# Kernel tuning notes

Measured on AMD Instinct MI355X. Metric: run time of the kernel, lower is better.

The kernel has to match this reference:

```python
import jax, jax.numpy as jnp
import numpy as np
import math

EMBED = 1024
HEADS = 16
HEAD_DIM = 64
HIDDEN = 4 * EMBED
EPS = 1e-5


def setup_inputs() -> dict:
    key = jax.random.key(0)
    ks = jax.random.split(key, 12)
    B, T, C = 2, 2048, EMBED
    s = 0.02
    return {
        "x": jax.random.normal(ks[0], (B, T, C), jnp.float32),
        "ln1_g": jnp.ones((C,), jnp.float32),
        "ln1_b": jnp.zeros((C,), jnp.float32),
        "qkv_w": jax.random.normal(ks[1], (C, 3 * C), jnp.float32) * s,
        "qkv_b": jnp.zeros((3 * C,), jnp.float32),
        "out_w": jax.random.normal(ks[2], (C, C), jnp.float32) * s,
        "out_b": jnp.zeros((C,), jnp.float32),
        "ln2_g": jnp.ones((C,), jnp.float32),
        "ln2_b": jnp.zeros((C,), jnp.float32),
        "fc1_w": jax.random.normal(ks[3], (C, HIDDEN), jnp.float32) * s,
        "fc1_b": jnp.zeros((HIDDEN,), jnp.float32),
        "fc2_w": jax.random.normal(ks[4], (HIDDEN, C), jnp.float32) * s,
        "fc2_b": jnp.zeros((C,), jnp.float32),
    }


def _layernorm(x, g, b):
    mu = jnp.mean(x, axis=-1, keepdims=True)
    var = jnp.var(x, axis=-1, keepdims=True)
    return (x - mu) * jax.lax.rsqrt(var + EPS) * g + b


def _attention(x, qkv_w, qkv_b, out_w, out_b):
    B, T, C = x.shape
    qkv = x @ qkv_w + qkv_b  # [B,T,3C]
    q, k, v = jnp.split(qkv, 3, axis=-1)
    # [B,H,T,hd]
    def heads(t):
        return t.reshape(B, T, HEADS, HEAD_DIM).transpose(0, 2, 1, 3)
    q, k, v = heads(q), heads(k), heads(v)
    scale = 1.0 / math.sqrt(HEAD_DIM)
    attn = jnp.einsum('bhqd,bhkd->bhqk', q, k) * scale
    causal = jnp.triu(jnp.ones((T, T), bool), k=1)
    attn = jnp.where(causal, -jnp.inf, attn)
    attn = jax.nn.softmax(attn, axis=-1)
    out = jnp.einsum('bhqk,bhkd->bhqd', attn, v)
    out = out.transpose(0, 2, 1, 3).reshape(B, T, C)
    return out @ out_w + out_b


def reference(x, ln1_g, ln1_b, qkv_w, qkv_b, out_w, out_b, ln2_g, ln2_b, fc1_w, fc1_b, fc2_w, fc2_b):
    x = x + _attention(_layernorm(x, ln1_g, ln1_b), qkv_w, qkv_b, out_w, out_b)
    h = _layernorm(x, ln2_g, ln2_b)
    h = jax.nn.gelu(h @ fc1_w + fc1_b, approximate=False) @ fc2_w + fc2_b
    return x + h
```

## Files before the change

kernel.cpp:

```cpp
#include <hip/hip_runtime.h>
#include <hip/hip_bf16.h>
#include <math.h>

typedef float f32x4 __attribute__((ext_vector_type(4)));
typedef __bf16 bf16x8 __attribute__((ext_vector_type(8)));
typedef __hip_bfloat16 bf16;

constexpr int T_SEQ = 2048;
constexpr int C_EMB = 1024;
constexpr int N_HEAD = 16;
constexpr int D_HEAD = 64;
constexpr int BATCH = 2;
constexpr int M_ROWS = BATCH * T_SEQ;
constexpr int HIDDEN_DIM = 4096;

static __device__ __forceinline__ f32x4 zero4() {
  f32x4 z; z[0] = 0.f; z[1] = 0.f; z[2] = 0.f; z[3] = 0.f; return z;
}

static __device__ __forceinline__ void gl_lds16(const bf16* g, bf16* l) {
  __builtin_amdgcn_global_load_lds(
      (const __attribute__((address_space(1))) unsigned int*)g,
      (__attribute__((address_space(3))) unsigned int*)l, 16, 0, 0);
}

__global__ __launch_bounds__(256) void ln_kernel(const float* __restrict__ x,
                                                 const float* __restrict__ gamma,
                                                 const float* __restrict__ beta,
                                                 bf16* __restrict__ out) {
  int row = blockIdx.x;
  const float* xr = x + (size_t)row * C_EMB;
  int t = threadIdx.x;
  float4 v = *(const float4*)&xr[t * 4];
  float s = v.x + v.y + v.z + v.w;
  float ss = v.x * v.x + v.y * v.y + v.z * v.z + v.w * v.w;
#pragma unroll
  for (int off = 32; off > 0; off >>= 1) {
    s += __shfl_down(s, off, 64);
    ss += __shfl_down(ss, off, 64);
  }
  __shared__ float sbuf[8];
  int w = t >> 6;
  if ((t & 63) == 0) { sbuf[w] = s; sbuf[4 + w] = ss; }
  __syncthreads();
  s = sbuf[0] + sbuf[1] + sbuf[2] + sbuf[3];
  ss = sbuf[4] + sbuf[5] + sbuf[6] + sbuf[7];
  float mu = s * (1.0f / C_EMB);
  float var = ss * (1.0f / C_EMB) - mu * mu;
  float rstd = rsqrtf(var + 1e-5f);
  float4 g4 = *(const float4*)&gamma[t * 4];
  float4 b4 = *(const float4*)&beta[t * 4];
  bf16* orow = out + (size_t)row * C_EMB + t * 4;
  orow[0] = __float2bfloat16((v.x - mu) * rstd * g4.x + b4.x);
  orow[1] = __float2bfloat16((v.y - mu) * rstd * g4.y + b4.y);
  orow[2] = __float2bfloat16((v.z - mu) * rstd * g4.z + b4.z);
  orow[3] = __float2bfloat16((v.w - mu) * rstd * g4.w + b4.w);
}

__global__ __launch_bounds__(256) void ln_red(const float* __restrict__ p0,
                                              const float* __restrict__ p1,
                                              const float* __restrict__ bias,
                                              const float* __restrict__ res,
                                              const float* __restrict__ gamma,
                                              const float* __restrict__ beta,
                                              float* __restrict__ x2,
                                              bf16* __restrict__ xb) {
  int row = blockIdx.x;
  int t = threadIdx.x;
  size_t base = (size_t)row * C_EMB + t * 4;
  float4 a = *(const float4*)&p0[base];
  float4 b = *(const float4*)&p1[base];
  float4 r = *(const float4*)&res[base];
  float4 bi = *(const float4*)&bias[t * 4];
  float4 v;
  v.x = a.x + b.x + r.x + bi.x;
  v.y = a.y + b.y + r.y + bi.y;
  v.z = a.z + b.z + r.z + bi.z;
  v.w = a.w + b.w + r.w + bi.w;
  *(float4*)&x2[base] = v;
  float s = v.x + v.y + v.z + v.w;
  float ss = v.x * v.x + v.y * v.y + v.z * v.z + v.w * v.w;
#pragma unroll
  for (int off = 32; off > 0; off >>= 1) {
    s += __shfl_down(s, off, 64);
    ss += __shfl_down(ss, off, 64);
  }
  __shared__ float sbuf[8];
  int w = t >> 6;
  if ((t & 63) == 0) { sbuf[w] = s; sbuf[4 + w] = ss; }
  __syncthreads();
  s = sbuf[0] + sbuf[1] + sbuf[2] + sbuf[3];
  ss = sbuf[4] + sbuf[5] + sbuf[6] + sbuf[7];
  float mu = s * (1.0f / C_EMB);
  float var = ss * (1.0f / C_EMB) - mu * mu;
  float rstd = rsqrtf(var + 1e-5f);
  float4 g4 = *(const float4*)&gamma[t * 4];
  float4 b4 = *(const float4*)&beta[t * 4];
  bf16* orow = xb + base;
  orow[0] = __float2bfloat16((v.x - mu) * rstd * g4.x + b4.x);
  orow[1] = __float2bfloat16((v.y - mu) * rstd * g4.y + b4.y);
  orow[2] = __float2bfloat16((v.z - mu) * rstd * g4.z + b4.z);
  orow[3] = __float2bfloat16((v.w - mu) * rstd * g4.w + b4.w);
}

__global__ __launch_bounds__(256) void cast_transpose(const float* __restrict__ src,
                                                      bf16* __restrict__ dst,
                                                      int K, int N) {
  __shared__ float tile[32][33];
  int n0 = blockIdx.x * 32, k0 = blockIdx.y * 32;
  int tx = threadIdx.x & 31, ty = threadIdx.x >> 5;
#pragma unroll
  for (int i = 0; i < 4; ++i)
    tile[ty + 8 * i][tx] = src[(size_t)(k0 + ty + 8 * i) * N + n0 + tx];
  __syncthreads();
#pragma unroll
  for (int i = 0; i < 4; ++i)
    dst[(size_t)(n0 + ty + 8 * i) * K + k0 + tx] = __float2bfloat16(tile[tx][ty + 8 * i]);
}

__global__ __launch_bounds__(256) void transpose_v(const bf16* __restrict__ V,
                                                   bf16* __restrict__ Vt) {
  int tt = blockIdx.x, bh = blockIdx.y;
  __shared__ bf16 tile[64][72];
  const bf16* src = V + ((size_t)bh * T_SEQ + tt * 64) * 64;
  int t = threadIdx.x;
  for (int idx = t; idx < 512; idx += 256) {
    int r = idx >> 3, c = (idx & 7) * 8;
    *(int4*)&tile[r][c] = *(const int4*)&src[r * 64 + c];
  }
  __syncthreads();
  bf16* dst = Vt + ((size_t)bh * 64) * T_SEQ + tt * 64;
  for (int idx = t; idx < 512; idx += 256) {
    int d = idx >> 3, c = (idx & 7) * 8;
    union { bf16 h[8]; int4 v; } u;
#pragma unroll
    for (int j = 0; j < 8; ++j) u.h[j] = tile[c + j][d];
    *(int4*)&dst[(size_t)d * T_SEQ + c] = u.v;
  }
}

template <int EPI, int BN>
__global__ __launch_bounds__(512) void gemm256(
    const bf16* __restrict__ A, const bf16* __restrict__ Bt,
    const float* __restrict__ bias, int M, int N, int K, int ksplit,
    bf16* __restrict__ out_b16,
    bf16* __restrict__ q_out, bf16* __restrict__ k_out, bf16* __restrict__ v_out,
    float* __restrict__ part0, float* __restrict__ part1) {
  constexpr int NFR = BN / 64;
  constexpr int NB = BN / 64;
  __shared__ bf16 Abuf[2][256 * 64];
  __shared__ bf16 Bbuf[2][BN * 64];

  int gx = gridDim.x, nwg = gx * gridDim.y;
  int flat = blockIdx.y * gx + blockIdx.x;
  int swz = (flat & 7) * (nwg >> 3) + (flat >> 3);
  int bx = swz % gx, by = swz / gx;

  int m0 = by * 256, n0 = bx * BN;
  int t = threadIdx.x;
  int wv = t >> 6, lane = t & 63, g = lane >> 4, r16 = lane & 15;
  int wm = wv >> 2, wn = wv & 3;

  f32x4 acc[8][NFR];
#pragma unroll
  for (int i = 0; i < 8; ++i)
#pragma unroll
    for (int j = 0; j < NFR; ++j) acc[i][j] = zero4();

  int srow = wv * 8 + (lane >> 3);
  int srcg = (lane & 7) ^ (lane >> 3);

  int klen = K / ksplit;
  int kbeg = blockIdx.z * klen;
  int NT = klen / 64;

  const bf16* gAp[4];
  const bf16* gBp[NB];
#pragma unroll
  for (int i = 0; i < 4; ++i)
    gAp[i] = A + (size_t)(m0 + i * 64 + srow) * K + kbeg + srcg * 8;
#pragma unroll
  for (int i = 0; i < NB; ++i)
    gBp[i] = Bt + (size_t)(n0 + i * 64 + srow) * K + kbeg + srcg * 8;

  int aoff[8], boff[NFR], xk[2];
#pragma unroll
  for (int mi = 0; mi < 8; ++mi) aoff[mi] = (wm * 128 + mi * 16 + r16) * 64;
#pragma unroll
  for (int ni = 0; ni < NFR; ++ni) boff[ni] = (wn * NFR * 16 + ni * 16 + r16) * 64;
#pragma unroll
  for (int kk = 0; kk < 2; ++kk) xk[kk] = (((kk * 4 + g) ^ (r16 & 7)) << 3);

  auto stage = [&](int buf) {
#pragma unroll
    for (int i = 0; i < 4; ++i) {
      gl_lds16(gAp[i], &Abuf[buf][(i * 64 + wv * 8) * 64]);
      gAp[i] += 64;
    }
#pragma unroll
    for (int i = 0; i < NB; ++i) {
      gl_lds16(gBp[i], &Bbuf[buf][(i * 64 + wv * 8) * 64]);
      gBp[i] += 64;
    }
  };

  auto compute = [&](int buf) {
    const bf16* Ab = &Abuf[buf][0];
    const bf16* Bb = &Bbuf[buf][0];
    bf16x8 bfr[NFR][2];
#pragma unroll
    for (int ni = 0; ni < NFR; ++ni)
#pragma unroll
      for (int kk = 0; kk < 2; ++kk)
        bfr[ni][kk] = *(const bf16x8*)&Bb[boff[ni] + xk[kk]];
    bf16x8 aa[2][2];
#pragma unroll
    for (int kk = 0; kk < 2; ++kk) aa[0][kk] = *(const bf16x8*)&Ab[aoff[0] + xk[kk]];
#pragma unroll
    for (int mi = 0; mi < 8; ++mi) {
      if (mi + 1 < 8) {
#pragma unroll
        for (int kk = 0; kk < 2; ++kk)
          aa[(mi + 1) & 1][kk] = *(const bf16x8*)&Ab[aoff[mi + 1] + xk[kk]];
      }
#pragma unroll
      for (int ni = 0; ni < NFR; ++ni) {
        acc[mi][ni] = __builtin_amdgcn_mfma_f32_16x16x32_bf16(aa[mi & 1][0], bfr[ni][0], acc[mi][ni], 0, 0, 0);
        acc[mi][ni] = __builtin_amdgcn_mfma_f32_16x16x32_bf16(aa[mi & 1][1], bfr[ni][1], acc[mi][ni], 0, 0, 0);
      }
    }
  };

  stage(0);
  __syncthreads();
  for (int tt = 0; tt < NT; ++tt) {
    int cur = tt & 1;
    if (tt + 1 < NT) stage(cur ^ 1);
    compute(cur);
    __syncthreads();
  }

  float* pout = (EPI == 3) ? (blockIdx.z == 0 ? part0 : part1) : nullptr;

#pragma unroll
  for (int mi = 0; mi < 8; ++mi) {
#pragma unroll
    for (int ni = 0; ni < NFR; ++ni) {
      int col = n0 + wn * NFR * 16 + ni * 16 + r16;
      float bv = (EPI == 3) ? 0.0f : bias[col];
#pragma unroll
      for (int reg = 0; reg < 4; ++reg) {
        int row = m0 + wm * 128 + mi * 16 + g * 4 + reg;
        float v = acc[mi][ni][reg] + bv;
        if constexpr (EPI == 0) {
          int part = col >> 10, cc = col & 1023;
          int hh = cc >> 6, dd = cc & 63;
          int bb = row >> 11, tt2 = row & 2047;
          size_t idx = (((size_t)bb * N_HEAD + hh) * T_SEQ + tt2) * D_HEAD + dd;
          if (part == 0) q_out[idx] = __float2bfloat16(v * 0.125f);
          else if (part == 1) k_out[idx] = __float2bfloat16(v);
          else v_out[idx] = __float2bfloat16(v);
        } else if constexpr (EPI == 2) {
          float ge = 0.5f * v * (1.0f + erff(v * 0.70710678118f));
          out_b16[(size_t)row * N + col] = __float2bfloat16(ge);
        } else {
          pout[(size_t)row * N + col] = v;
        }
      }
    }
  }
}

__global__ __launch_bounds__(256) void reduce_add(const float* __restrict__ p0,
                                                  const float* __restrict__ p1,
                                                  const float* __restrict__ bias,
                                                  const float* __restrict__ res,
                                                  float* __restrict__ out,
                                                  int total, int N) {
  for (int i = (blockIdx.x * 256 + threadIdx.x) * 4; i < total; i += gridDim.x * 1024) {
    float4 a = *(const float4*)&p0[i];
    float4 b = *(const float4*)&p1[i];
    float4 r = *(const float4*)&res[i];
    float4 bi = *(const float4*)&bias[i & (N - 1)];
    float4 o;
    o.x = a.x + b.x + r.x + bi.x;
    o.y = a.y + b.y + r.y + bi.y;
    o.z = a.z + b.z + r.z + bi.z;
    o.w = a.w + b.w + r.w + bi.w;
    *(float4*)&out[i] = o;
  }
}

__global__ __launch_bounds__(256) void attn_kernel(const bf16* __restrict__ Q,
                                                   const bf16* __restrict__ Kg,
                                                   const bf16* __restrict__ Vt,
                                                   bf16* __restrict__ O) {
  constexpr int NQ = T_SEQ / 64;
  int p = blockIdx.x, bh = blockIdx.y;
  int qtA = p, qtB = NQ - 1 - p;
  int b = bh >> 4, h = bh & 15;
  __shared__ bf16 Ks[2][64 * 64];
  __shared__ bf16 Vs[2][64 * 64];
  __shared__ bf16 Ps[4][16 * 64];
  int t = threadIdx.x, w = t >> 6, lane = t & 63, g = lane >> 4, r16 = lane & 15;

  const bf16* QpA = Q + ((size_t)bh * T_SEQ + qtA * 64) * 64;
  const bf16* QpB = Q + ((size_t)bh * T_SEQ + qtB * 64) * 64;
  bf16x8 qfA[2], qfB[2];
#pragma unroll
  for (int kk = 0; kk < 2; ++kk) {
    qfA[kk] = *(const bf16x8*)&QpA[(w * 16 + r16) * 64 + kk * 32 + g * 8];
    qfB[kk] = *(const bf16x8*)&QpB[(w * 16 + r16) * 64 + kk * 32 + g * 8];
  }

  float lsA[4] = {0.f, 0.f, 0.f, 0.f}, lsB[4] = {0.f, 0.f, 0.f, 0.f};
  f32x4 oA[4], oB[4];
#pragma unroll
  for (int i = 0; i < 4; ++i) { oA[i] = zero4(); oB[i] = zero4(); }

  bf16* Psw = Ps[w];

  int sg0 = w * 128 + lane, sg1 = w * 128 + 64 + lane;
  int sr0 = sg0 >> 3, sc0 = (sg0 & 7) ^ (sr0 & 7);
  int sr1 = sg1 >> 3, sc1 = (sg1 & 7) ^ (sr1 & 7);

  auto stage = [&](int kt, int buf) {
    const bf16* Kp = Kg + ((size_t)bh * T_SEQ + kt * 64) * 64;
    const bf16* Vp = Vt + (size_t)bh * 64 * T_SEQ + kt * 64;
    gl_lds16(Kp + sr0 * 64 + sc0 * 8, &Ks[buf][(w * 128) * 8]);
    gl_lds16(Vp + (size_t)sr0 * T_SEQ + sc0 * 8, &Vs[buf][(w * 128) * 8]);
    gl_lds16(Kp + sr1 * 64 + sc1 * 8, &Ks[buf][(w * 128 + 64) * 8]);
    gl_lds16(Vp + (size_t)sr1 * T_SEQ + sc1 * 8, &Vs[buf][(w * 128 + 64) * 8]);
  };

  auto process = [&](const bf16x8* qf, float* ls, f32x4* o_acc, bool diag,
                     const bf16* Ksb, const bf16* Vsb) {
    f32x4 s[4];
#pragma unroll
    for (int ni = 0; ni < 4; ++ni) {
      s[ni] = zero4();
#pragma unroll
      for (int kk = 0; kk < 2; ++kk) {
        bf16x8 kf = *(const bf16x8*)&Ksb[(ni * 16 + r16) * 64 + (((kk * 4 + g) ^ (r16 & 7)) << 3)];
        s[ni] = __builtin_amdgcn_mfma_f32_16x16x32_bf16(qf[kk], kf, s[ni], 0, 0, 0);
      }
    }
    if (diag) {
#pragma unroll
      for (int ni = 0; ni < 4; ++ni) {
        int kl = ni * 16 + r16;
#pragma unroll
        for (int reg = 0; reg < 4; ++reg) {
          int ql = w * 16 + g * 4 + reg;
          if (kl > ql) s[ni][reg] = -1e30f;
        }
      }
    }
#pragma unroll
    for (int ni = 0; ni < 4; ++ni) {
#pragma unroll
      for (int reg = 0; reg < 4; ++reg) {
        float pv = __expf(s[ni][reg]);
        s[ni][reg] = pv;
        ls[reg] += pv;
        int rr = g * 4 + reg;
        Psw[rr * 64 + (((ni * 2 + (r16 >> 3)) ^ (rr & 7)) << 3) + (r16 & 7)] =
            __float2bfloat16(pv);
      }
    }
    bf16x8 pf[2];
#pragma unroll
    for (int kk = 0; kk < 2; ++kk)
      pf[kk] = *(const bf16x8*)&Psw[r16 * 64 + (((kk * 4 + g) ^ (r16 & 7)) << 3)];
#pragma unroll
    for (int nd = 0; nd < 4; ++nd)
#pragma unroll
      for (int kk = 0; kk < 2; ++kk) {
        bf16x8 vf = *(const bf16x8*)&Vsb[(nd * 16 + r16) * 64 + (((kk * 4 + g) ^ (r16 & 7)) << 3)];
        o_acc[nd] = __builtin_amdgcn_mfma_f32_16x16x32_bf16(pf[kk], vf, o_acc[nd], 0, 0, 0);
      }
  };

  stage(0, 0);
  __syncthreads();
  for (int kt = 0; kt <= qtB; ++kt) {
    int cur = kt & 1;
    if (kt + 1 <= qtB) stage(kt + 1, cur ^ 1);
    process(qfB, lsB, oB, kt == qtB, &Ks[cur][0], &Vs[cur][0]);
    if (kt <= qtA) process(qfA, lsA, oA, kt == qtA, &Ks[cur][0], &Vs[cur][0]);
    __syncthreads();
  }

#pragma unroll
  for (int reg = 0; reg < 4; ++reg) {
#pragma unroll
    for (int off = 1; off < 16; off <<= 1) {
      lsA[reg] += __shfl_xor(lsA[reg], off, 64);
      lsB[reg] += __shfl_xor(lsB[reg], off, 64);
    }
  }
#pragma unroll
  for (int reg = 0; reg < 4; ++reg) {
    float invA = 1.0f / lsA[reg];
    float invB = 1.0f / lsB[reg];
    int rowA = b * T_SEQ + qtA * 64 + w * 16 + g * 4 + reg;
    int rowB = b * T_SEQ + qtB * 64 + w * 16 + g * 4 + reg;
#pragma unroll
    for (int nd = 0; nd < 4; ++nd) {
      int col = h * 64 + nd * 16 + r16;
      O[(size_t)rowA * C_EMB + col] = __float2bfloat16(oA[nd][reg] * invA);
      O[(size_t)rowB * C_EMB + col] = __float2bfloat16(oB[nd][reg] * invB);
    }
  }
}

extern "C" void kernel_launch(void* const* d_in, const int* in_sizes, int n_in,
                              void* d_out, int out_size, void* d_ws, size_t ws_size,
                              hipStream_t stream) {
  (void)in_sizes; (void)n_in; (void)out_size; (void)ws_size;
  const float* x     = (const float*)d_in[0];
  const float* ln1_g = (const float*)d_in[1];
  const float* ln1_b = (const float*)d_in[2];
  const float* qkv_w = (const float*)d_in[3];
  const float* qkv_b = (const float*)d_in[4];
  const float* out_w = (const float*)d_in[5];
  const float* out_b = (const float*)d_in[6];
  const float* ln2_g = (const float*)d_in[7];
  const float* ln2_b = (const float*)d_in[8];
  const float* fc1_w = (const float*)d_in[9];
  const float* fc1_b = (const float*)d_in[10];
  const float* fc2_w = (const float*)d_in[11];
  const float* fc2_b = (const float*)d_in[12];
  float* out = (float*)d_out;

  char* ws = (char*)d_ws;
  size_t off = 0;
  auto alloc = [&](size_t bytes) {
    void* p = ws + off;
    off += (bytes + 255) & ~(size_t)255;
    return p;
  };
  bf16* Wqkv = (bf16*)alloc((size_t)3 * C_EMB * C_EMB * 2);
  bf16* Wout = (bf16*)alloc((size_t)C_EMB * C_EMB * 2);
  bf16* W1   = (bf16*)alloc((size_t)HIDDEN_DIM * C_EMB * 2);
  bf16* W2   = (bf16*)alloc((size_t)C_EMB * HIDDEN_DIM * 2);
  float* x2  = (float*)alloc((size_t)M_ROWS * C_EMB * 4);
  bf16* Xb   = (bf16*)alloc((size_t)M_ROWS * C_EMB * 2);
  bf16* Qb   = (bf16*)alloc((size_t)M_ROWS * C_EMB * 2 * 4);
  bf16* Kb   = Qb + (size_t)M_ROWS * C_EMB;
  bf16* Vb   = Kb + (size_t)M_ROWS * C_EMB;
  bf16* Vtb  = Vb + (size_t)M_ROWS * C_EMB;
  bf16* H1   = Qb;
  float* p0o = (float*)Qb;
  float* p1o = (float*)Vb;
  float* p0f = (float*)Wqkv;
  float* p1f = (float*)alloc((size_t)M_ROWS * C_EMB * 4);

  cast_transpose<<<dim3(3 * C_EMB / 32, C_EMB / 32), 256, 0, stream>>>(qkv_w, Wqkv, C_EMB, 3 * C_EMB);
  cast_transpose<<<dim3(C_EMB / 32, C_EMB / 32), 256, 0, stream>>>(out_w, Wout, C_EMB, C_EMB);
  cast_transpose<<<dim3(HIDDEN_DIM / 32, C_EMB / 32), 256, 0, stream>>>(fc1_w, W1, C_EMB, HIDDEN_DIM);
  cast_transpose<<<dim3(C_EMB / 32, HIDDEN_DIM / 32), 256, 0, stream>>>(fc2_w, W2, HIDDEN_DIM, C_EMB);

  ln_kernel<<<M_ROWS, 256, 0, stream>>>(x, ln1_g, ln1_b, Xb);

  gemm256<0, 256><<<dim3(3 * C_EMB / 256, M_ROWS / 256), 512, 0, stream>>>(
      Xb, Wqkv, qkv_b, M_ROWS, 3 * C_EMB, C_EMB, 1,
      nullptr, Qb, Kb, Vb, nullptr, nullptr);

  transpose_v<<<dim3(T_SEQ / 64, BATCH * N_HEAD), 256, 0, stream>>>(Vb, Vtb);

  attn_kernel<<<dim3(T_SEQ / 128, BATCH * N_HEAD), 256, 0, stream>>>(Qb, Kb, Vtb, Xb);

  gemm256<3, 128><<<dim3(C_EMB / 128, M_ROWS / 256, 2), 512, 0, stream>>>(
      Xb, Wout, nullptr, M_ROWS, C_EMB, C_EMB, 2,
      nullptr, nullptr, nullptr, nullptr, p0o, p1o);
  ln_red<<<M_ROWS, 256, 0, stream>>>(p0o, p1o, out_b, x, ln2_g, ln2_b, x2, Xb);

  gemm256<2, 256><<<dim3(HIDDEN_DIM / 256, M_ROWS / 256), 512, 0, stream>>>(
      Xb, W1, fc1_b, M_ROWS, HIDDEN_DIM, C_EMB, 1,
      H1, nullptr, nullptr, nullptr, nullptr, nullptr);

  gemm256<3, 128><<<dim3(C_EMB / 128, M_ROWS / 256, 2), 512, 0, stream>>>(
      H1, W2, nullptr, M_ROWS, C_EMB, HIDDEN_DIM, 2,
      nullptr, nullptr, nullptr, nullptr, p0f, p1f);
  reduce_add<<<2048, 256, 0, stream>>>(p0f, p1f, fc2_b, x2, out,
                                       M_ROWS * C_EMB, C_EMB);
}
```

Before: 243.7 us.

## Use explicit vmcnt waits and split barriers to overlap prefetch with compute

Replaces the __syncthreads-based double-buffer loops in the GEMM and attention kernels with raw s_barrier calls, sched_barrier fences, and s_waitcnt vmcnt(N). This lets the next tile's global-to-LDS loads stay in flight while the current tile is computed, instead of draining every outstanding load at each barrier. It also raises wave priority during GEMM compute. The risk is correctness: the vmcnt counts must exactly match the number of loads issued per stage, or data races on LDS can occur.

Measured after the change: 254.7 us. +4.5%, slower.

```diff
diff --git a/kernel.cpp b/kernel.cpp
--- a/kernel.cpp
+++ b/kernel.cpp
@@ -148,6 +148,7 @@
     float* __restrict__ part0, float* __restrict__ part1) {
   constexpr int NFR = BN / 64;
   constexpr int NB = BN / 64;
+  constexpr int LOADS = 4 + NB;
   __shared__ bf16 Abuf[2][256 * 64];
   __shared__ bf16 Bbuf[2][BN * 64];
 
@@ -232,12 +233,22 @@
   };
 
   stage(0);
-  __syncthreads();
   for (int tt = 0; tt < NT; ++tt) {
     int cur = tt & 1;
-    if (tt + 1 < NT) stage(cur ^ 1);
+    __builtin_amdgcn_s_barrier();
+    __builtin_amdgcn_sched_barrier(0);
+    if (tt + 1 < NT) {
+      stage(cur ^ 1);
+      asm volatile("s_waitcnt vmcnt(%0)" :: "n"(LOADS) : "memory");
+    } else {
+      asm volatile("s_waitcnt vmcnt(0)" ::: "memory");
+    }
+    __builtin_amdgcn_sched_barrier(0);
+    __builtin_amdgcn_s_barrier();
+    __builtin_amdgcn_sched_barrier(0);
+    __builtin_amdgcn_s_setprio(1);
     compute(cur);
-    __syncthreads();
+    __builtin_amdgcn_s_setprio(0);
   }
 
   float* pout = (EPI == 3) ? (blockIdx.z == 0 ? part0 : part1) : nullptr;
@@ -382,13 +393,21 @@
   };
 
   stage(0, 0);
-  __syncthreads();
   for (int kt = 0; kt <= qtB; ++kt) {
     int cur = kt & 1;
-    if (kt + 1 <= qtB) stage(kt + 1, cur ^ 1);
+    __builtin_amdgcn_s_barrier();
+    __builtin_amdgcn_sched_barrier(0);
+    if (kt + 1 <= qtB) {
+      stage(kt + 1, cur ^ 1);
+      asm volatile("s_waitcnt vmcnt(4)" ::: "memory");
+    } else {
+      asm volatile("s_waitcnt vmcnt(0)" ::: "memory");
+    }
+    __builtin_amdgcn_sched_barrier(0);
+    __builtin_amdgcn_s_barrier();
+    __builtin_amdgcn_sched_barrier(0);
     process(qfB, lsB, oB, kt == qtB, &Ks[cur][0], &Vs[cur][0]);
     if (kt <= qtA) process(qfA, lsA, oA, kt == qtA, &Ks[cur][0], &Vs[cur][0]);
-    __syncthreads();
   }
 
 #pragma unroll
```

## Restructure GEMM into 8-phase half-tile pipeline with fine-grained barriers

Applied to the files above, without the earlier changes.

Replaces the double-buffered GEMM main loop with an 8-phase schedule. A and B tiles are split into halves that are staged one at a time, interleaved with MFMA sub-blocks, and guarded by explicit vmcnt waits and raw s_barrier. s_setprio is raised around the MFMA bursts. The goal is to overlap global-to-LDS loads with compute more evenly and to cut full-tile sync stalls. The cost is more barriers, and correctness now relies on the exact vmcnt counts.

After: 276.3 us. 13.4% more time.

```diff
diff --git a/kernel.cpp b/kernel.cpp
--- a/kernel.cpp
+++ b/kernel.cpp
@@ -23,6 +23,8 @@
       (const __attribute__((address_space(1))) unsigned int*)g,
       (__attribute__((address_space(3))) unsigned int*)l, 16, 0, 0);
 }
+
+#define BAR() asm volatile("s_barrier" ::: "memory")
 
 __global__ __launch_bounds__(256) void ln_kernel(const float* __restrict__ x,
                                                  const float* __restrict__ gamma,
@@ -140,16 +142,16 @@
 }
 
 template <int EPI, int BN>
-__global__ __launch_bounds__(512) void gemm256(
+__global__ __launch_bounds__(512) void gemm8p(
     const bf16* __restrict__ A, const bf16* __restrict__ Bt,
     const float* __restrict__ bias, int M, int N, int K, int ksplit,
     bf16* __restrict__ out_b16,
     bf16* __restrict__ q_out, bf16* __restrict__ k_out, bf16* __restrict__ v_out,
     float* __restrict__ part0, float* __restrict__ part1) {
   constexpr int NFR = BN / 64;
-  constexpr int NB = BN / 64;
-  __shared__ bf16 Abuf[2][256 * 64];
-  __shared__ bf16 Bbuf[2][BN * 64];
+  constexpr int BH = BN / 2;
+  __shared__ bf16 Asl[2][2][128 * 64];
+  __shared__ bf16 Bsl[2][2][BH * 64];
 
   int gx = gridDim.x, nwg = gx * gridDim.y;
   int flat = blockIdx.y * gx + blockIdx.x;
@@ -167,77 +169,93 @@
 #pragma unroll
     for (int j = 0; j < NFR; ++j) acc[i][j] = zero4();
 
-  int srow = wv * 8 + (lane >> 3);
-  int srcg = (lane & 7) ^ (lane >> 3);
+  int lrow8 = lane >> 3;
+  int srcg = (lane & 7) ^ lrow8;
 
   int klen = K / ksplit;
   int kbeg = blockIdx.z * klen;
   int NT = klen / 64;
-
-  const bf16* gAp[4];
-  const bf16* gBp[NB];
-#pragma unroll
-  for (int i = 0; i < 4; ++i)
-    gAp[i] = A + (size_t)(m0 + i * 64 + srow) * K + kbeg + srcg * 8;
-#pragma unroll
-  for (int i = 0; i < NB; ++i)
-    gBp[i] = Bt + (size_t)(n0 + i * 64 + srow) * K + kbeg + srcg * 8;
-
-  int aoff[8], boff[NFR], xk[2];
-#pragma unroll
-  for (int mi = 0; mi < 8; ++mi) aoff[mi] = (wm * 128 + mi * 16 + r16) * 64;
-#pragma unroll
-  for (int ni = 0; ni < NFR; ++ni) boff[ni] = (wn * NFR * 16 + ni * 16 + r16) * 64;
+  int NI = NT / 2;
+
+  auto stageA = [&](int tile, int h) {
+    int par = tile & 1;
+    const bf16* base = A + (size_t)(m0 + h * 128) * K + kbeg + tile * 64;
+#pragma unroll
+    for (int j = 0; j < 2; ++j) {
+      const bf16* src = base + (size_t)((wv * 2 + j) * 8 + lrow8) * K + srcg * 8;
+      gl_lds16(src, &Asl[par][h][((wv * 2 + j) * 8) * 64]);
+    }
+  };
+  auto stageB = [&](int tile, int h) {
+    int par = tile & 1;
+    const bf16* base = Bt + (size_t)(n0 + h * BH) * K + kbeg + tile * 64;
+    if constexpr (BN == 256) {
+#pragma unroll
+      for (int j = 0; j < 2; ++j) {
+        const bf16* src = base + (size_t)((wv * 2 + j) * 8 + lrow8) * K + srcg * 8;
+        gl_lds16(src, &Bsl[par][h][((wv * 2 + j) * 8) * 64]);
+      }
+    } else {
+      const bf16* src = base + (size_t)(wv * 8 + lrow8) * K + srcg * 8;
+      gl_lds16(src, &Bsl[par][h][(wv * 8) * 64]);
+    }
+  };
+
+  int xk[2];
 #pragma unroll
   for (int kk = 0; kk < 2; ++kk) xk[kk] = (((kk * 4 + g) ^ (r16 & 7)) << 3);
-
-  auto stage = [&](int buf) {
-#pragma unroll
-    for (int i = 0; i < 4; ++i) {
-      gl_lds16(gAp[i], &Abuf[buf][(i * 64 + wv * 8) * 64]);
-      gAp[i] += 64;
-    }
-#pragma unroll
-    for (int i = 0; i < NB; ++i) {
-      gl_lds16(gBp[i], &Bbuf[buf][(i * 64 + wv * 8) * 64]);
-      gBp[i] += 64;
-    }
-  };
-
-  auto compute = [&](int buf) {
-    const bf16* Ab = &Abuf[buf][0];
-    const bf16* Bb = &Bbuf[buf][0];
-    bf16x8 bfr[NFR][2];
-#pragma unroll
-    for (int ni = 0; ni < NFR; ++ni)
-#pragma unroll
-      for (int kk = 0; kk < 2; ++kk)
-        bfr[ni][kk] = *(const bf16x8*)&Bb[boff[ni] + xk[kk]];
-    bf16x8 aa[2][2];
-#pragma unroll
-    for (int kk = 0; kk < 2; ++kk) aa[0][kk] = *(const bf16x8*)&Ab[aoff[0] + xk[kk]];
-#pragma unroll
-    for (int mi = 0; mi < 8; ++mi) {
-      if (mi + 1 < 8) {
+  int bhalf = wn >> 1;
+  int blrow0 = (wn & 1) * 16 * NFR;
+
+  stageA(0, 0); stageA(0, 1); stageB(0, 0); stageB(0, 1);
+
+  bf16x8 bfr[NFR][2];
+
+  for (int it = 0; it < NI; ++it) {
+    int e = 2 * it, o = 2 * it + 1;
+#pragma unroll
+    for (int p = 0; p < 8; ++p) {
+      int stile = (p < 4) ? o : (e + 2);
+      int sh = p & 3;
+      bool staged = (stile < NT);
+      if (staged) {
+        if (sh < 2) stageA(stile, sh); else stageB(stile, sh - 2);
+      }
+      if ((p & 3) == 0) {
+        if (staged)
+          asm volatile("s_waitcnt vmcnt(2)" ::: "memory");
+        else
+          asm volatile("s_waitcnt vmcnt(0)" ::: "memory");
+        BAR();
+      }
+      int par = (p < 4) ? 0 : 1;
+      int q = p & 3;
+      const bf16* Ab = &Asl[par][wm][0];
+      const bf16* Bb = &Bsl[par][bhalf][0];
+      __builtin_amdgcn_s_setprio(1);
+      if (q == 0) {
+#pragma unroll
+        for (int ni = 0; ni < NFR; ++ni)
+#pragma unroll
+          for (int kk = 0; kk < 2; ++kk)
+            bfr[ni][kk] = *(const bf16x8*)&Bb[(blrow0 + ni * 16 + r16) * 64 + xk[kk]];
+      }
+      bf16x8 af[2][2];
+#pragma unroll
+      for (int d = 0; d < 2; ++d)
 #pragma unroll
         for (int kk = 0; kk < 2; ++kk)
-          aa[(mi + 1) & 1][kk] = *(const bf16x8*)&Ab[aoff[mi + 1] + xk[kk]];
-      }
-#pragma unroll
-      for (int ni = 0; ni < NFR; ++ni) {
-        acc[mi][ni] = __builtin_amdgcn_mfma_f32_16x16x32_bf16(aa[mi & 1][0], bfr[ni][0], acc[mi][ni], 0, 0, 0);
-        acc[mi][ni] = __builtin_amdgcn_mfma_f32_16x16x32_bf16(aa[mi & 1][1], bfr[ni][1], acc[mi][ni], 0, 0, 0);
-      }
-    }
-  };
-
-  stage(0);
-  __syncthreads();
-  for (int tt = 0; tt < NT; ++tt) {
-    int cur = tt & 1;
-    if (tt + 1 < NT) stage(cur ^ 1);
-    compute(cur);
-    __syncthreads();
+          af[d][kk] = *(const bf16x8*)&Ab[((2 * q + d) * 16 + r16) * 64 + xk[kk]];
+#pragma unroll
+      for (int d = 0; d < 2; ++d)
+#pragma unroll
+        for (int ni = 0; ni < NFR; ++ni) {
+          acc[2 * q + d][ni] = __builtin_amdgcn_mfma_f32_16x16x32_bf16(af[d][0], bfr[ni][0], acc[2 * q + d][ni], 0, 0, 0);
+          acc[2 * q + d][ni] = __builtin_amdgcn_mfma_f32_16x16x32_bf16(af[d][1], bfr[ni][1], acc[2 * q + d][ni], 0, 0, 0);
+        }
+      __builtin_amdgcn_s_setprio(0);
+      BAR();
+    }
   }
 
   float* pout = (EPI == 3) ? (blockIdx.z == 0 ? part0 : part1) : nullptr;
@@ -463,7 +481,7 @@
 
   ln_kernel<<<M_ROWS, 256, 0, stream>>>(x, ln1_g, ln1_b, Xb);
 
-  gemm256<0, 256><<<dim3(3 * C_EMB / 256, M_ROWS / 256), 512, 0, stream>>>(
+  gemm8p<0, 256><<<dim3(3 * C_EMB / 256, M_ROWS / 256), 512, 0, stream>>>(
       Xb, Wqkv, qkv_b, M_ROWS, 3 * C_EMB, C_EMB, 1,
       nullptr, Qb, Kb, Vb, nullptr, nullptr);
 
@@ -471,16 +489,16 @@
 
   attn_kernel<<<dim3(T_SEQ / 128, BATCH * N_HEAD), 256, 0, stream>>>(Qb, Kb, Vtb, Xb);
 
-  gemm256<3, 128><<<dim3(C_EMB / 128, M_ROWS / 256, 2), 512, 0, stream>>>(
+  gemm8p<3, 128><<<dim3(C_EMB / 128, M_ROWS / 256, 2), 512, 0, stream>>>(
       Xb, Wout, nullptr, M_ROWS, C_EMB, C_EMB, 2,
       nullptr, nullptr, nullptr, nullptr, p0o, p1o);
   ln_red<<<M_ROWS, 256, 0, stream>>>(p0o, p1o, out_b, x, ln2_g, ln2_b, x2, Xb);
 
-  gemm256<2, 256><<<dim3(HIDDEN_DIM / 256, M_ROWS / 256), 512, 0, stream>>>(
+  gemm8p<2, 256><<<dim3(HIDDEN_DIM / 256, M_ROWS / 256), 512, 0, stream>>>(
       Xb, W1, fc1_b, M_ROWS, HIDDEN_DIM, C_EMB, 1,
       H1, nullptr, nullptr, nullptr, nullptr, nullptr);
 
-  gemm256<3, 128><<<dim3(C_EMB / 128, M_ROWS / 256, 2), 512, 0, stream>>>(
+  gemm8p<3, 128><<<dim3(C_EMB / 128, M_ROWS / 256, 2), 512, 0, stream>>>(
       H1, W2, nullptr, M_ROWS, C_EMB, HIDDEN_DIM, 2,
       nullptr, nullptr, nullptr, nullptr, p0f, p1f);
   reduce_add<<<2048, 256, 0, stream>>>(p0f, p1f, fc2_b, x2, out,
```

## Add finely pipelined 256x256 GEMM for QKV and FC1 projections

Applied to the files above, without the earlier changes.

Adds a new GEMM kernel for the QKV and FC1 projections that splits the A and B tiles into 128-row halves and interleaves their global-to-LDS loads across four compute sub-phases. B is prefetched two k-tiles ahead, with explicit vmcnt waits, raw s_barriers and setprio around the MFMA bursts. The goal is to hide load latency better than the old stage-then-compute loop with its full syncthreads. The hand-tuned waitcnt counts are fragile, and the per-quarter barriers add sync overhead.

Measured after the change: 246.4 us. No clear change (+1.1%).

```diff
diff --git a/kernel.cpp b/kernel.cpp
--- a/kernel.cpp
+++ b/kernel.cpp
@@ -23,6 +23,8 @@
       (const __attribute__((address_space(1))) unsigned int*)g,
       (__attribute__((address_space(3))) unsigned int*)l, 16, 0, 0);
 }
+
+#define BAR() asm volatile("s_barrier" ::: "memory")
 
 __global__ __launch_bounds__(256) void ln_kernel(const float* __restrict__ x,
                                                  const float* __restrict__ gamma,
@@ -139,24 +141,22 @@
   }
 }
 
-template <int EPI, int BN>
-__global__ __launch_bounds__(512) void gemm256(
+template <int EPI>
+__global__ __launch_bounds__(512) void gemm8p(
     const bf16* __restrict__ A, const bf16* __restrict__ Bt,
-    const float* __restrict__ bias, int M, int N, int K, int ksplit,
+    const float* __restrict__ bias, int M, int N, int K,
     bf16* __restrict__ out_b16,
-    bf16* __restrict__ q_out, bf16* __restrict__ k_out, bf16* __restrict__ v_out,
-    float* __restrict__ part0, float* __restrict__ part1) {
-  constexpr int NFR = BN / 64;
-  constexpr int NB = BN / 64;
-  __shared__ bf16 Abuf[2][256 * 64];
-  __shared__ bf16 Bbuf[2][BN * 64];
+    bf16* __restrict__ q_out, bf16* __restrict__ k_out, bf16* __restrict__ v_out) {
+  constexpr int NFR = 4;
+  __shared__ bf16 Asl[2][2][128 * 64];
+  __shared__ bf16 Bsl[2][2][128 * 64];
 
   int gx = gridDim.x, nwg = gx * gridDim.y;
   int flat = blockIdx.y * gx + blockIdx.x;
   int swz = (flat & 7) * (nwg >> 3) + (flat >> 3);
   int bx = swz % gx, by = swz / gx;
 
-  int m0 = by * 256, n0 = bx * BN;
+  int m0 = by * 256, n0 = bx * 256;
   int t = threadIdx.x;
   int wv = t >> 6, lane = t & 63, g = lane >> 4, r16 = lane & 15;
   int wm = wv >> 2, wn = wv & 3;
@@ -167,87 +167,97 @@
 #pragma unroll
     for (int j = 0; j < NFR; ++j) acc[i][j] = zero4();
 
-  int srow = wv * 8 + (lane >> 3);
-  int srcg = (lane & 7) ^ (lane >> 3);
-
-  int klen = K / ksplit;
-  int kbeg = blockIdx.z * klen;
-  int NT = klen / 64;
-
-  const bf16* gAp[4];
-  const bf16* gBp[NB];
-#pragma unroll
-  for (int i = 0; i < 4; ++i)
-    gAp[i] = A + (size_t)(m0 + i * 64 + srow) * K + kbeg + srcg * 8;
-#pragma unroll
-  for (int i = 0; i < NB; ++i)
-    gBp[i] = Bt + (size_t)(n0 + i * 64 + srow) * K + kbeg + srcg * 8;
-
-  int aoff[8], boff[NFR], xk[2];
-#pragma unroll
-  for (int mi = 0; mi < 8; ++mi) aoff[mi] = (wm * 128 + mi * 16 + r16) * 64;
-#pragma unroll
-  for (int ni = 0; ni < NFR; ++ni) boff[ni] = (wn * NFR * 16 + ni * 16 + r16) * 64;
+  int lrow8 = lane >> 3;
+  int srcg = (lane & 7) ^ lrow8;
+  int NT = K / 64;
+
+  auto stageA = [&](int tile, int h) {
+    int par = tile & 1;
+    const bf16* base = A + (size_t)(m0 + h * 128) * K + tile * 64;
+#pragma unroll
+    for (int j = 0; j < 2; ++j) {
+      const bf16* src = base + (size_t)((wv * 2 + j) * 8 + lrow8) * K + srcg * 8;
+      gl_lds16(src, &Asl[par][h][((wv * 2 + j) * 8) * 64]);
+    }
+  };
+  auto stageB = [&](int tile, int h) {
+    int par = tile & 1;
+    const bf16* base = Bt + (size_t)(n0 + h * 128) * K + tile * 64;
+#pragma unroll
+    for (int j = 0; j < 2; ++j) {
+      const bf16* src = base + (size_t)((wv * 2 + j) * 8 + lrow8) * K + srcg * 8;
+      gl_lds16(src, &Bsl[par][h][((wv * 2 + j) * 8) * 64]);
+    }
+  };
+
+  int xk[2];
 #pragma unroll
   for (int kk = 0; kk < 2; ++kk) xk[kk] = (((kk * 4 + g) ^ (r16 & 7)) << 3);
-
-  auto stage = [&](int buf) {
-#pragma unroll
-    for (int i = 0; i < 4; ++i) {
-      gl_lds16(gAp[i], &Abuf[buf][(i * 64 + wv * 8) * 64]);
-      gAp[i] += 64;
-    }
-#pragma unroll
-    for (int i = 0; i < NB; ++i) {
-      gl_lds16(gBp[i], &Bbuf[buf][(i * 64 + wv * 8) * 64]);
-      gBp[i] += 64;
-    }
-  };
-
-  auto compute = [&](int buf) {
-    const bf16* Ab = &Abuf[buf][0];
-    const bf16* Bb = &Bbuf[buf][0];
-    bf16x8 bfr[NFR][2];
-#pragma unroll
-    for (int ni = 0; ni < NFR; ++ni)
-#pragma unroll
-      for (int kk = 0; kk < 2; ++kk)
-        bfr[ni][kk] = *(const bf16x8*)&Bb[boff[ni] + xk[kk]];
-    bf16x8 aa[2][2];
-#pragma unroll
-    for (int kk = 0; kk < 2; ++kk) aa[0][kk] = *(const bf16x8*)&Ab[aoff[0] + xk[kk]];
-#pragma unroll
-    for (int mi = 0; mi < 8; ++mi) {
-      if (mi + 1 < 8) {
+  int bhalf = wn >> 1;
+  int blrow0 = (wn & 1) * 64;
+
+  stageA(0, 0); stageA(0, 1); stageB(0, 0); stageB(0, 1);
+  if (NT > 1) {
+    stageB(1, 0); stageB(1, 1);
+    asm volatile("s_waitcnt vmcnt(4)" ::: "memory");
+  } else {
+    asm volatile("s_waitcnt vmcnt(0)" ::: "memory");
+  }
+  BAR();
+
+  bf16x8 bfr[NFR][2];
+
+  for (int u = 0; u < NT; ++u) {
+    int par = u & 1;
+    const bf16* Ab = &Asl[par][wm][0];
+    const bf16* Bb = &Bsl[par][bhalf][0];
+#pragma unroll
+    for (int q = 0; q < 4; ++q) {
+      if (q == 0) {
+#pragma unroll
+        for (int ni = 0; ni < NFR; ++ni)
+#pragma unroll
+          for (int kk = 0; kk < 2; ++kk)
+            bfr[ni][kk] = *(const bf16x8*)&Bb[(blrow0 + ni * 16 + r16) * 64 + xk[kk]];
+      }
+      bf16x8 af[2][2];
+#pragma unroll
+      for (int d = 0; d < 2; ++d)
 #pragma unroll
         for (int kk = 0; kk < 2; ++kk)
-          aa[(mi + 1) & 1][kk] = *(const bf16x8*)&Ab[aoff[mi + 1] + xk[kk]];
-      }
-#pragma unroll
-      for (int ni = 0; ni < NFR; ++ni) {
-        acc[mi][ni] = __builtin_amdgcn_mfma_f32_16x16x32_bf16(aa[mi & 1][0], bfr[ni][0], acc[mi][ni], 0, 0, 0);
-        acc[mi][ni] = __builtin_amdgcn_mfma_f32_16x16x32_bf16(aa[mi & 1][1], bfr[ni][1], acc[mi][ni], 0, 0, 0);
-      }
-    }
-  };
-
-  stage(0);
-  __syncthreads();
-  for (int tt = 0; tt < NT; ++tt) {
-    int cur = tt & 1;
-    if (tt + 1 < NT) stage(cur ^ 1);
-    compute(cur);
-    __syncthreads();
-  }
-
-  float* pout = (EPI == 3) ? (blockIdx.z == 0 ? part0 : part1) : nullptr;
+          af[d][kk] = *(const bf16x8*)&Ab[((2 * q + d) * 16 + r16) * 64 + xk[kk]];
+      if (q == 0) { if (u + 1 < NT) stageA(u + 1, 0); }
+      else if (q == 1) { if (u + 1 < NT) stageA(u + 1, 1); }
+      else if (q == 2) { if (u + 2 < NT) stageB(u + 2, 0); }
+      else { if (u + 2 < NT) stageB(u + 2, 1); }
+      BAR();
+      asm volatile("s_waitcnt lgkmcnt(0)" ::: "memory");
+      __builtin_amdgcn_sched_barrier(0);
+      __builtin_amdgcn_s_setprio(1);
+#pragma unroll
+      for (int d = 0; d < 2; ++d)
+#pragma unroll
+        for (int ni = 0; ni < NFR; ++ni) {
+          acc[2 * q + d][ni] = __builtin_amdgcn_mfma_f32_16x16x32_bf16(af[d][0], bfr[ni][0], acc[2 * q + d][ni], 0, 0, 0);
+          acc[2 * q + d][ni] = __builtin_amdgcn_mfma_f32_16x16x32_bf16(af[d][1], bfr[ni][1], acc[2 * q + d][ni], 0, 0, 0);
+        }
+      __builtin_amdgcn_s_setprio(0);
+      if (q == 3) {
+        if (u + 2 < NT)
+          asm volatile("s_waitcnt vmcnt(4)" ::: "memory");
+        else
+          asm volatile("s_waitcnt vmcnt(0)" ::: "memory");
+      }
+      BAR();
+    }
+  }
 
 #pragma unroll
   for (int mi = 0; mi < 8; ++mi) {
 #pragma unroll
     for (int ni = 0; ni < NFR; ++ni) {
-      int col = n0 + wn * NFR * 16 + ni * 16 + r16;
-      float bv = (EPI == 3) ? 0.0f : bias[col];
+      int col = n0 + wn * 64 + ni * 16 + r16;
+      float bv = bias[col];
 #pragma unroll
       for (int reg = 0; reg < 4; ++reg) {
         int row = m0 + wm * 128 + mi * 16 + g * 4 + reg;
@@ -260,15 +270,130 @@
           if (part == 0) q_out[idx] = __float2bfloat16(v * 0.125f);
           else if (part == 1) k_out[idx] = __float2bfloat16(v);
           else v_out[idx] = __float2bfloat16(v);
-        } else if constexpr (EPI == 2) {
+        } else {
           float ge = 0.5f * v * (1.0f + erff(v * 0.70710678118f));
           out_b16[(size_t)row * N + col] = __float2bfloat16(ge);
-        } else {
-          pout[(size_t)row * N + col] = v;
         }
       }
     }
   }
+}
+
+template <int EPI, int BN>
+__global__ __launch_bounds__(512) void gemm256(
+    const bf16* __restrict__ A, const bf16* __restrict__ Bt,
+    const float* __restrict__ bias, int M, int N, int K, int ksplit,
+    bf16* __restrict__ out_b16,
+    float* __restrict__ part0, float* __restrict__ part1) {
+  constexpr int NFR = BN / 64;
+  constexpr int NB = BN / 64;
+  __shared__ bf16 Abuf[2][256 * 64];
+  __shared__ bf16 Bbuf[2][BN * 64];
+
+  int gx = gridDim.x, nwg = gx * gridDim.y;
+  int flat = blockIdx.y * gx + blockIdx.x;
+  int swz = (flat & 7) * (nwg >> 3) + (flat >> 3);
+  int bx = swz % gx, by = swz / gx;
+
+  int m0 = by * 256, n0 = bx * BN;
+  int t = threadIdx.x;
+  int wv = t >> 6, lane = t & 63, g = lane >> 4, r16 = lane & 15;
+  int wm = wv >> 2, wn = wv & 3;
+
+  f32x4 acc[8][NFR];
+#pragma unroll
+  for (int i = 0; i < 8; ++i)
+#pragma unroll
+    for (int j = 0; j < NFR; ++j) acc[i][j] = zero4();
+
+  int srow = wv * 8 + (lane >> 3);
+  int srcg = (lane & 7) ^ (lane >> 3);
+
+  int klen = K / ksplit;
+  int kbeg = blockIdx.z * klen;
+  int NT = klen / 64;
+
+  const bf16* gAp[4];
+  const bf16* gBp[NB];
+#pragma unroll
+  for (int i = 0; i < 4; ++i)
+    gAp[i] = A + (size_t)(m0 + i * 64 + srow) * K + kbeg + srcg * 8;
+#pragma unroll
+  for (int i = 0; i < NB; ++i)
+    gBp[i] = Bt + (size_t)(n0 + i * 64 + srow) * K + kbeg + srcg * 8;
+
+  int aoff[8], boff[NFR], xk[2];
+#pragma unroll
+  for (int mi = 0; mi < 8; ++mi) aoff[mi] = (wm * 128 + mi * 16 + r16) * 64;
+#pragma unroll
+  for (int ni = 0; ni < NFR; ++ni) boff[ni] = (wn * NFR * 16 + ni * 16 + r16) * 64;
+#pragma unroll
+  for (int kk = 0; kk < 2; ++kk) xk[kk] = (((kk * 4 + g) ^ (r16 & 7)) << 3);
+
+  auto stage = [&](int buf) {
+#pragma unroll
+    for (int i = 0; i < 4; ++i) {
+      gl_lds16(gAp[i], &Abuf[buf][(i * 64 + wv * 8) * 64]);
+      gAp[i] += 64;
+    }
+#pragma unroll
+    for (int i = 0; i < NB; ++i) {
+      gl_lds16(gBp[i], &Bbuf[buf][(i * 64 + wv * 8) * 64]);
+      gBp[i] += 64;
+    }
+  };
+
+  auto compute = [&](int buf) {
+    const bf16* Ab = &Abuf[buf][0];
+    const bf16* Bb = &Bbuf[buf][0];
+    bf16x8 bfr[NFR][2];
+#pragma unroll
+    for (int ni = 0; ni < NFR; ++ni)
+#pragma unroll
+      for (int kk = 0; kk < 2; ++kk)
+        bfr[ni][kk] = *(const bf16x8*)&Bb[boff[ni] + xk[kk]];
+    bf16x8 aa[2][2];
+#pragma unroll
+    for (int kk = 0; kk < 2; ++kk) aa[0][kk] = *(const bf16x8*)&Ab[aoff[0] + xk[kk]];
+#pragma unroll
+    for (int mi = 0; mi < 8; ++mi) {
+      if (mi + 1 < 8) {
+#pragma unroll
+        for (int kk = 0; kk < 2; ++kk)
+          aa[(mi + 1) & 1][kk] = *(const bf16x8*)&Ab[aoff[mi + 1] + xk[kk]];
+      }
+#pragma unroll
+      for (int ni = 0; ni < NFR; ++ni) {
+        acc[mi][ni] = __builtin_amdgcn_mfma_f32_16x16x32_bf16(aa[mi & 1][0], bfr[ni][0], acc[mi][ni], 0, 0, 0);
+        acc[mi][ni] = __builtin_amdgcn_mfma_f32_16x16x32_bf16(aa[mi & 1][1], bfr[ni][1], acc[mi][ni], 0, 0, 0);
+      }
+    }
+  };
+
+  stage(0);
+  __syncthreads();
+  for (int tt = 0; tt < NT; ++tt) {
+    int cur = tt & 1;
+    if (tt + 1 < NT) stage(cur ^ 1);
+    compute(cur);
+    __syncthreads();
+  }
+
+  float* pout = (blockIdx.z == 0) ? part0 : part1;
+
+#pragma unroll
+  for (int mi = 0; mi < 8; ++mi) {
+#pragma unroll
+    for (int ni = 0; ni < NFR; ++ni) {
+      int col = n0 + wn * NFR * 16 + ni * 16 + r16;
+#pragma unroll
+      for (int reg = 0; reg < 4; ++reg) {
+        int row = m0 + wm * 128 + mi * 16 + g * 4 + reg;
+        pout[(size_t)row * N + col] = acc[mi][ni][reg];
+      }
+    }
+  }
+  (void)bias; (void)out_b16;
 }
 
 __global__ __launch_bounds__(256) void reduce_add(const float* __restrict__ p0,
@@ -463,9 +588,9 @@
 
   ln_kernel<<<M_ROWS, 256, 0, stream>>>(x, ln1_g, ln1_b, Xb);
 
-  gemm256<0, 256><<<dim3(3 * C_EMB / 256, M_ROWS / 256), 512, 0, stream>>>(
-      Xb, Wqkv, qkv_b, M_ROWS, 3 * C_EMB, C_EMB, 1,
-      nullptr, Qb, Kb, Vb, nullptr, nullptr);
+  gemm8p<0><<<dim3(3 * C_EMB / 256, M_ROWS / 256), 512, 0, stream>>>(
+      Xb, Wqkv, qkv_b, M_ROWS, 3 * C_EMB, C_EMB,
+      nullptr, Qb, Kb, Vb);
 
   transpose_v<<<dim3(T_SEQ / 64, BATCH * N_HEAD), 256, 0, stream>>>(Vb, Vtb);
 
@@ -473,16 +598,16 @@
 
   gemm256<3, 128><<<dim3(C_EMB / 128, M_ROWS / 256, 2), 512, 0, stream>>>(
       Xb, Wout, nullptr, M_ROWS, C_EMB, C_EMB, 2,
-      nullptr, nullptr, nullptr, nullptr, p0o, p1o);
+      nullptr, p0o, p1o);
   ln_red<<<M_ROWS, 256, 0, stream>>>(p0o, p1o, out_b, x, ln2_g, ln2_b, x2, Xb);
 
-  gemm256<2, 256><<<dim3(HIDDEN_DIM / 256, M_ROWS / 256), 512, 0, stream>>>(
-      Xb, W1, fc1_b, M_ROWS, HIDDEN_DIM, C_EMB, 1,
-      H1, nullptr, nullptr, nullptr, nullptr, nullptr);
+  gemm8p<2><<<dim3(HIDDEN_DIM / 256, M_ROWS / 256), 512, 0, stream>>>(
+      Xb, W1, fc1_b, M_ROWS, HIDDEN_DIM, C_EMB,
+      H1, nullptr, nullptr, nullptr);
 
   gemm256<3, 128><<<dim3(C_EMB / 128, M_ROWS / 256, 2), 512, 0, stream>>>(
       H1, W2, nullptr, M_ROWS, C_EMB, HIDDEN_DIM, 2,
-      nullptr, nullptr, nullptr, nullptr, p0f, p1f);
+      nullptr, p0f, p1f);
   reduce_add<<<2048, 256, 0, stream>>>(p0f, p1f, fc2_b, x2, out,
                                        M_ROWS * C_EMB, C_EMB);
 }
```
